# Performance work log

Hardware: AMD Instinct MI355X
Metric: run time of the kernel (lower is better)

## Reference

```python
import jax, jax.numpy as jnp
import numpy as np

B = 16384
N_NARR = 128
N_SUB = 1024
K = N_SUB // N_NARR  # narrative i -> subnarratives [i*K, (i+1)*K)
GAMMA = 2.0
NW, SW, HW = 1.0, 1.0, 0.5  # narrative/subnarrative/hierarchy weights


def setup_inputs() -> dict:
    key = jax.random.key(0)
    k1, k2, k3, k4 = jax.random.split(key, 4)
    return {
        "narrative_logits": jax.random.normal(k1, (B, N_NARR), jnp.float32),
        "subnarrative_logits": jax.random.normal(k2, (B, N_SUB), jnp.float32),
        "narrative_labels": jax.random.randint(k3, (B, N_NARR), 0, 2, jnp.int32),
        "subnarrative_labels": jax.random.randint(k4, (B, N_SUB), 0, 2, jnp.int32),
    }


def _weighted_bce(logits, labels, pos_weight):
    # BCEWithLogits with pos_weight: pw*y*softplus(-x) + (1-y)*softplus(x)
    return pos_weight * labels * jax.nn.softplus(-logits) + (1.0 - labels) * jax.nn.softplus(logits)


def reference(narrative_logits, subnarrative_logits, narrative_labels, subnarrative_labels):
    nl = narrative_labels.astype(jnp.float32)
    sl = subnarrative_labels.astype(jnp.float32)
    b = narrative_logits.shape[0]

    # class-balanced pos_weights, clamped to [1, 50]
    npw = jnp.clip((1.0 - nl).sum(0) / (nl.sum(0) + 1e-6), 1.0, 50.0)
    spw = jnp.clip((1.0 - sl).sum(0) / (sl.sum(0) + 1e-6), 1.0, 50.0)

    narrative_loss = _weighted_bce(narrative_logits, nl, npw).mean()

    # ragged subnarrative loss, vectorized: groups of K subnarrs per narrative.
    # per-(sample, positive-narrative) mean BCE over the group, averaged over
    # the number of valid (sample, narrative) pairs -- same math as the loop.
    sub_bce = _weighted_bce(subnarrative_logits, sl, spw).reshape(b, N_NARR, K)
    per_group = sub_bce.mean(-1)              # [B, N_NARR]
    pos = nl                                   # positive-narrative mask [B, N_NARR]
    valid_count = pos.sum()
    subnarrative_loss = jnp.where(
        valid_count > 0, (per_group * pos).sum() / jnp.maximum(valid_count, 1.0), 0.0)

    # hierarchy consistency: relu(max subnarr prob - narr prob) over positives
    nprob = jax.nn.sigmoid(narrative_logits)
    sprob = jax.nn.sigmoid(subnarrative_logits)
    grp_max = sprob.reshape(b, N_NARR, K).max(-1)  # [B, N_NARR]
    hierarchy_loss = (jax.nn.relu(grp_max - nprob) * pos).sum() / b

    # focal terms (mean over all elements)
    nf = ((1.0 - nprob) ** GAMMA * nl * jax.nn.log_sigmoid(narrative_logits)).mean()
    sf = ((1.0 - sprob) ** GAMMA * sl * jax.nn.log_sigmoid(subnarrative_logits)).mean()

    total = (NW * (narrative_loss - 0.1 * nf)
             + SW * (subnarrative_loss - 0.1 * sf)
             + HW * hierarchy_loss)
    return total
```

## Files before the change

### kernel.cpp

```cpp
#include <hip/hip_runtime.h>


#define BDIM 256
#define NROWS 16384
#define NNARR 128
#define NSUB 1024

#define WS_AN    0
#define WS_CN    128
#define WS_NSUM  256
#define WS_AS    384
#define WS_CS    1408
#define WS_SSUM  2432
#define WS_FN    3456
#define WS_FS    3457
#define WS_HIER  3458
#define WS_FLOATS 3459
#define CSTRIDE  3472

#define NCHUNK 32

__device__ __forceinline__ void bce_pieces(float x, float& sp_p, float& sp_m, float& sig) {
    float a = fabsf(x);
    float e = __expf(-a);
    float l = __logf(1.0f + e);
    sp_p = fmaxf(x, 0.0f) + l;
    sp_m = sp_p - x;
    float inv = __builtin_amdgcn_rcpf(1.0f + e);
    sig = (x >= 0.0f) ? inv : e * inv;
}

template<int RPB>
__global__ __launch_bounds__(BDIM, 6) void ncl_main(
    const float* __restrict__ nlog, const float* __restrict__ slog,
    const int*   __restrict__ nlab, const int*   __restrict__ slab,
    float* __restrict__ P)
{
    __shared__ float sred[BDIM][13];
    __shared__ float ssc[4][3];

    const int t  = threadIdx.x;
    const int r0 = blockIdx.x * RPB;
    float* const Pb = P + (size_t)blockIdx.x * CSTRIDE;

    float fn = 0.f, fs = 0.f, hier = 0.f;

    {
        float An[4] = {0,0,0,0}, Cn[4] = {0,0,0,0}, ns[4] = {0,0,0,0};
        #pragma unroll
        for (int i = 0; i < RPB / 8; ++i) {
            const int base = r0 * NNARR + 4 * (i * BDIM + t);
            const float4 xs = *(const float4*)(nlog + base);
            const int4   ys = *(const int4*)  (nlab + base);
            const float xv[4] = {xs.x, xs.y, xs.z, xs.w};
            const float yv[4] = {(float)ys.x, (float)ys.y, (float)ys.z, (float)ys.w};
            #pragma unroll
            for (int j = 0; j < 4; ++j) {
                float sp_p, sp_m, sig;
                bce_pieces(xv[j], sp_p, sp_m, sig);
                float y = yv[j];
                An[j] += y * sp_m;
                Cn[j] += (1.0f - y) * sp_p;
                ns[j] += y;
                float om = 1.0f - sig;
                fn += om * om * y * (-sp_m);
            }
        }
        #pragma unroll
        for (int j = 0; j < 4; ++j) {
            sred[t][j] = An[j]; sred[t][4 + j] = Cn[j]; sred[t][8 + j] = ns[j];
        }
    }
    __syncthreads();
    if (t < 32) {
        float a[12];
        #pragma unroll
        for (int j = 0; j < 12; ++j) a[j] = sred[t][j];
        #pragma unroll
        for (int s = 1; s < 8; ++s)
            #pragma unroll
            for (int j = 0; j < 12; ++j) a[j] += sred[t + 32 * s][j];
        *(float4*)(Pb + WS_AN   + 4 * t) = make_float4(a[0], a[1], a[2],  a[3]);
        *(float4*)(Pb + WS_CN   + 4 * t) = make_float4(a[4], a[5], a[6],  a[7]);
        *(float4*)(Pb + WS_NSUM + 4 * t) = make_float4(a[8], a[9], a[10], a[11]);
    }

    const int g = t >> 1;
    float As[4] = {0,0,0,0}, Cs[4] = {0,0,0,0}, ss[4] = {0,0,0,0};
    #pragma unroll 4
    for (int i = 0; i < RPB; ++i) {
        const int r = r0 + i;
        const float  nx   = nlog[r * NNARR + g];
        const float  posv = (float)nlab[r * NNARR + g];
        const float4 xs = *(const float4*)(slog + (size_t)r * NSUB + 4 * t);
        const int4   ys = *(const int4*)  (slab + (size_t)r * NSUB + 4 * t);

        float nsig;
        {
            float a = fabsf(nx);
            float e = __expf(-a);
            float inv = __builtin_amdgcn_rcpf(1.0f + e);
            nsig = (nx >= 0.0f) ? inv : e * inv;
        }

        const float xv[4] = {xs.x, xs.y, xs.z, xs.w};
        const float yv[4] = {(float)ys.x, (float)ys.y, (float)ys.z, (float)ys.w};
        float mymax = 0.0f;
        #pragma unroll
        for (int j = 0; j < 4; ++j) {
            float sp_p, sp_m, sig;
            bce_pieces(xv[j], sp_p, sp_m, sig);
            float y = yv[j];
            As[j] += posv * y * sp_m;
            Cs[j] += posv * (1.0f - y) * sp_p;
            ss[j] += y;
            float om = 1.0f - sig;
            fs += om * om * y * (-sp_m);
            mymax = fmaxf(mymax, sig);
        }
        float gmax = fmaxf(mymax, __shfl_xor(mymax, 1, 64));
        if ((t & 1) == 0)
            hier += fmaxf(gmax - nsig, 0.0f) * posv;
    }

    *(float4*)(Pb + WS_AS   + 4 * t) = make_float4(As[0], As[1], As[2], As[3]);
    *(float4*)(Pb + WS_CS   + 4 * t) = make_float4(Cs[0], Cs[1], Cs[2], Cs[3]);
    *(float4*)(Pb + WS_SSUM + 4 * t) = make_float4(ss[0], ss[1], ss[2], ss[3]);

    #pragma unroll
    for (int off = 32; off; off >>= 1) {
        fn   += __shfl_down(fn,   off, 64);
        fs   += __shfl_down(fs,   off, 64);
        hier += __shfl_down(hier, off, 64);
    }
    if ((t & 63) == 0) {
        int w = t >> 6;
        ssc[w][0] = fn; ssc[w][1] = fs; ssc[w][2] = hier;
    }
    __syncthreads();
    if (t == 0) {
        float a = 0.f, b = 0.f, c = 0.f;
        #pragma unroll
        for (int w = 0; w < 4; ++w) { a += ssc[w][0]; b += ssc[w][1]; c += ssc[w][2]; }
        Pb[WS_FN] = a; Pb[WS_FS] = b; Pb[WS_HIER] = c;
    }
}

__global__ __launch_bounds__(256) void ncl_reduce1(const float* __restrict__ P,
                                                   float* __restrict__ tmp,
                                                   int tpg)
{
    const int e = blockIdx.x * 256 + threadIdx.x;
    if (e >= WS_FLOATS) return;
    const int g = blockIdx.y;
    const float* p = P + (size_t)g * tpg * CSTRIDE + e;
    float s = 0.f;
    #pragma unroll 4
    for (int i = 0; i < tpg; ++i)
        s += p[(size_t)i * CSTRIDE];
    tmp[(size_t)g * CSTRIDE + e] = s;
}

__global__ __launch_bounds__(1024) void ncl_finalize(const float* __restrict__ tmp,
                                                     float* __restrict__ out)
{
    __shared__ float sr[6][16];
    const int t = threadIdx.x;
    const float Bf = (float)NROWS;

    float As = 0.f, Csv = 0.f, ss = 0.f;
    #pragma unroll 4
    for (int gc = 0; gc < NCHUNK; ++gc) {
        const float* p = tmp + (size_t)gc * CSTRIDE;
        As  += p[WS_AS   + t];
        Csv += p[WS_CS   + t];
        ss  += p[WS_SSUM + t];
    }
    float spw = fminf(fmaxf((Bf - ss) / (ss + 1e-6f), 1.0f), 50.0f);
    float sub_part = spw * As + Csv;

    float narr_part = 0.f, valid_part = 0.f;
    if (t < NNARR) {
        float An = 0.f, Cn = 0.f, ns = 0.f;
        #pragma unroll 4
        for (int gc = 0; gc < NCHUNK; ++gc) {
            const float* p = tmp + (size_t)gc * CSTRIDE;
            An += p[WS_AN + t]; Cn += p[WS_CN + t]; ns += p[WS_NSUM + t];
        }
        float npw = fminf(fmaxf((Bf - ns) / (ns + 1e-6f), 1.0f), 50.0f);
        narr_part  = npw * An + Cn;
        valid_part = ns;
    }

    float fn_p = 0.f, fs_p = 0.f, hier_p = 0.f;
    if (t < NCHUNK) {
        const float* p = tmp + (size_t)t * CSTRIDE;
        fn_p = p[WS_FN]; fs_p = p[WS_FS]; hier_p = p[WS_HIER];
    }

    #pragma unroll
    for (int off = 32; off; off >>= 1) {
        sub_part   += __shfl_down(sub_part,   off, 64);
        narr_part  += __shfl_down(narr_part,  off, 64);
        valid_part += __shfl_down(valid_part, off, 64);
        fn_p       += __shfl_down(fn_p,       off, 64);
        fs_p       += __shfl_down(fs_p,       off, 64);
        hier_p     += __shfl_down(hier_p,     off, 64);
    }
    if ((t & 63) == 0) {
        int w = t >> 6;
        sr[0][w] = sub_part; sr[1][w] = narr_part; sr[2][w] = valid_part;
        sr[3][w] = fn_p;     sr[4][w] = fs_p;      sr[5][w] = hier_p;
    }
    __syncthreads();
    if (t == 0) {
        float sub_tot = 0.f, narr_tot = 0.f, valid = 0.f;
        float fn = 0.f, fs = 0.f, hier = 0.f;
        #pragma unroll
        for (int i = 0; i < 16; ++i) {
            sub_tot += sr[0][i]; narr_tot += sr[1][i]; valid += sr[2][i];
            fn += sr[3][i]; fs += sr[4][i]; hier += sr[5][i];
        }

        float narrative_loss = narr_tot / (Bf * (float)NNARR);
        float sub_loss = (valid > 0.0f) ? (sub_tot * (1.0f / 8.0f)) / fmaxf(valid, 1.0f) : 0.0f;
        float nf = fn / (Bf * (float)NNARR);
        float sf = fs / (Bf * (float)NSUB);
        float hier_loss = hier / Bf;

        out[0] = (narrative_loss - 0.1f * nf)
               + (sub_loss       - 0.1f * sf)
               + 0.5f * hier_loss;
    }
}

extern "C" void kernel_launch(void* const* d_in, const int* in_sizes, int n_in,
                              void* d_out, int out_size, void* d_ws, size_t ws_size,
                              hipStream_t stream) {
    const float* nlog = (const float*)d_in[0];
    const float* slog = (const float*)d_in[1];
    const int*   nlab = (const int*)d_in[2];
    const int*   slab = (const int*)d_in[3];
    float* P   = (float*)d_ws;
    float* out = (float*)d_out;

    const size_t availf = ws_size / 4;
    const bool big = availf >= (size_t)(2048 + NCHUNK) * CSTRIDE;
    const int nblocks = big ? 2048 : 1024;
    float* tmp = P + (size_t)nblocks * CSTRIDE;
    const int tpg = nblocks / NCHUNK;

    if (big)
        ncl_main<8><<<2048, BDIM, 0, stream>>>(nlog, slog, nlab, slab, P);
    else
        ncl_main<16><<<1024, BDIM, 0, stream>>>(nlog, slog, nlab, slab, P);

    dim3 gr((WS_FLOATS + 255) / 256, NCHUNK);
    ncl_reduce1<<<gr, 256, 0, stream>>>(P, tmp, tpg);
    ncl_finalize<<<1, 1024, 0, stream>>>(tmp, out);
}
```

Measured before the change: 186.3 us.

## Fuse narrative loss into per-row loop and batch four-row loads per iteration

The separate narrative-loss pass, along with its shared-memory reduction and barrier, is folded into the subnarrative row loop. Each even thread now computes the narrative BCE and focal terms for its group from the narrative logit it already loads. Each iteration issues loads for four rows up front to keep more memory requests in flight, and the grid is fixed at 1024 blocks of 16 rows with occupancy hint 4. This drops the redundant narrative transcendental work and the LDS reduction, at the cost of higher register pressure and less parallelism than the 2048-block path.

```diff
diff --git a/kernel.cpp b/kernel.cpp
--- a/kernel.cpp
+++ b/kernel.cpp
@@ -5,6 +5,8 @@
 #define NROWS 16384
 #define NNARR 128
 #define NSUB 1024
+#define RPB 16
+#define NBLOCKS (NROWS / RPB)
 
 #define WS_AN    0
 #define WS_CN    128
@@ -18,7 +20,8 @@
 #define WS_FLOATS 3459
 #define CSTRIDE  3472
 
-#define NCHUNK 32
+#define NCHUNK 16
+#define TPG (NBLOCKS / NCHUNK)
 
 __device__ __forceinline__ void bce_pieces(float x, float& sp_p, float& sp_m, float& sig) {
     float a = fabsf(x);
@@ -30,102 +33,92 @@
     sig = (x >= 0.0f) ? inv : e * inv;
 }
 
-template<int RPB>
-__global__ __launch_bounds__(BDIM, 6) void ncl_main(
+__device__ __forceinline__ void row_accum(
+    const float4 xs, const int4 ys, float nx, float posv, int t,
+    float As[4], float Cs[4], float ss[4],
+    float& An, float& Cn, float& ns, float& fn, float& fs, float& hier)
+{
+    float nsp_p, nsp_m, nsig;
+    bce_pieces(nx, nsp_p, nsp_m, nsig);
+
+    const float xv[4] = {xs.x, xs.y, xs.z, xs.w};
+    const float yv[4] = {(float)ys.x, (float)ys.y, (float)ys.z, (float)ys.w};
+    float mymax = 0.0f;
+    #pragma unroll
+    for (int k = 0; k < 4; ++k) {
+        float sp_p, sp_m, sig;
+        bce_pieces(xv[k], sp_p, sp_m, sig);
+        float y = yv[k];
+        As[k] += posv * y * sp_m;
+        Cs[k] += posv * (1.0f - y) * sp_p;
+        ss[k] += y;
+        float om = 1.0f - sig;
+        fs += om * om * y * (-sp_m);
+        mymax = fmaxf(mymax, sig);
+    }
+    float gmax = fmaxf(mymax, __shfl_xor(mymax, 1, 64));
+    if ((t & 1) == 0) {
+        hier += fmaxf(gmax - nsig, 0.0f) * posv;
+        An += posv * nsp_m;
+        Cn += (1.0f - posv) * nsp_p;
+        ns += posv;
+        float om = 1.0f - nsig;
+        fn += om * om * posv * (-nsp_m);
+    }
+}
+
+__global__ __launch_bounds__(BDIM, 4) void ncl_main(
     const float* __restrict__ nlog, const float* __restrict__ slog,
     const int*   __restrict__ nlab, const int*   __restrict__ slab,
     float* __restrict__ P)
 {
-    __shared__ float sred[BDIM][13];
     __shared__ float ssc[4][3];
 
     const int t  = threadIdx.x;
+    const int g  = t >> 1;
     const int r0 = blockIdx.x * RPB;
     float* const Pb = P + (size_t)blockIdx.x * CSTRIDE;
 
-    float fn = 0.f, fs = 0.f, hier = 0.f;
-
-    {
-        float An[4] = {0,0,0,0}, Cn[4] = {0,0,0,0}, ns[4] = {0,0,0,0};
-        #pragma unroll
-        for (int i = 0; i < RPB / 8; ++i) {
-            const int base = r0 * NNARR + 4 * (i * BDIM + t);
-            const float4 xs = *(const float4*)(nlog + base);
-            const int4   ys = *(const int4*)  (nlab + base);
-            const float xv[4] = {xs.x, xs.y, xs.z, xs.w};
-            const float yv[4] = {(float)ys.x, (float)ys.y, (float)ys.z, (float)ys.w};
-            #pragma unroll
-            for (int j = 0; j < 4; ++j) {
-                float sp_p, sp_m, sig;
-                bce_pieces(xv[j], sp_p, sp_m, sig);
-                float y = yv[j];
-                An[j] += y * sp_m;
-                Cn[j] += (1.0f - y) * sp_p;
-                ns[j] += y;
-                float om = 1.0f - sig;
-                fn += om * om * y * (-sp_m);
-            }
+    float As[4] = {0,0,0,0}, Cs[4] = {0,0,0,0}, ss[4] = {0,0,0,0};
+    float An = 0.f, Cn = 0.f, ns = 0.f, fn = 0.f, fs = 0.f, hier = 0.f;
+
+    #pragma unroll
+    for (int ii = 0; ii < RPB / 4; ++ii) {
+        float4 xs0, xs1, xs2, xs3;
+        int4   ys0, ys1, ys2, ys3;
+        float  nx0, nx1, nx2, nx3, pv0, pv1, pv2, pv3;
+        {
+            const int r = r0 + 4 * ii;
+            const float* s0 = slog + (size_t)r * NSUB + 4 * t;
+            const int*   l0 = slab + (size_t)r * NSUB + 4 * t;
+            const float* n0 = nlog + (size_t)r * NNARR + g;
+            const int*   m0 = nlab + (size_t)r * NNARR + g;
+            xs0 = *(const float4*)(s0);
+            xs1 = *(const float4*)(s0 + NSUB);
+            xs2 = *(const float4*)(s0 + 2 * NSUB);
+            xs3 = *(const float4*)(s0 + 3 * NSUB);
+            ys0 = *(const int4*)(l0);
+            ys1 = *(const int4*)(l0 + NSUB);
+            ys2 = *(const int4*)(l0 + 2 * NSUB);
+            ys3 = *(const int4*)(l0 + 3 * NSUB);
+            nx0 = n0[0]; nx1 = n0[NNARR]; nx2 = n0[2 * NNARR]; nx3 = n0[3 * NNARR];
+            pv0 = (float)m0[0];         pv1 = (float)m0[NNARR];
+            pv2 = (float)m0[2 * NNARR]; pv3 = (float)m0[3 * NNARR];
         }
-        #pragma unroll
-        for (int j = 0; j < 4; ++j) {
-            sred[t][j] = An[j]; sred[t][4 + j] = Cn[j]; sred[t][8 + j] = ns[j];
-        }
-    }
-    __syncthreads();
-    if (t < 32) {
-        float a[12];
-        #pragma unroll
-        for (int j = 0; j < 12; ++j) a[j] = sred[t][j];
-        #pragma unroll
-        for (int s = 1; s < 8; ++s)
-            #pragma unroll
-            for (int j = 0; j < 12; ++j) a[j] += sred[t + 32 * s][j];
-        *(float4*)(Pb + WS_AN   + 4 * t) = make_float4(a[0], a[1], a[2],  a[3]);
-        *(float4*)(Pb + WS_CN   + 4 * t) = make_float4(a[4], a[5], a[6],  a[7]);
-        *(float4*)(Pb + WS_NSUM + 4 * t) = make_float4(a[8], a[9], a[10], a[11]);
-    }
-
-    const int g = t >> 1;
-    float As[4] = {0,0,0,0}, Cs[4] = {0,0,0,0}, ss[4] = {0,0,0,0};
-    #pragma unroll 4
-    for (int i = 0; i < RPB; ++i) {
-        const int r = r0 + i;
-        const float  nx   = nlog[r * NNARR + g];
-        const float  posv = (float)nlab[r * NNARR + g];
-        const float4 xs = *(const float4*)(slog + (size_t)r * NSUB + 4 * t);
-        const int4   ys = *(const int4*)  (slab + (size_t)r * NSUB + 4 * t);
-
-        float nsig;
-        {
-            float a = fabsf(nx);
-            float e = __expf(-a);
-            float inv = __builtin_amdgcn_rcpf(1.0f + e);
-            nsig = (nx >= 0.0f) ? inv : e * inv;
-        }
-
-        const float xv[4] = {xs.x, xs.y, xs.z, xs.w};
-        const float yv[4] = {(float)ys.x, (float)ys.y, (float)ys.z, (float)ys.w};
-        float mymax = 0.0f;
-        #pragma unroll
-        for (int j = 0; j < 4; ++j) {
-            float sp_p, sp_m, sig;
-            bce_pieces(xv[j], sp_p, sp_m, sig);
-            float y = yv[j];
-            As[j] += posv * y * sp_m;
-            Cs[j] += posv * (1.0f - y) * sp_p;
-            ss[j] += y;
-            float om = 1.0f - sig;
-            fs += om * om * y * (-sp_m);
-            mymax = fmaxf(mymax, sig);
-        }
-        float gmax = fmaxf(mymax, __shfl_xor(mymax, 1, 64));
-        if ((t & 1) == 0)
-            hier += fmaxf(gmax - nsig, 0.0f) * posv;
+        row_accum(xs0, ys0, nx0, pv0, t, As, Cs, ss, An, Cn, ns, fn, fs, hier);
+        row_accum(xs1, ys1, nx1, pv1, t, As, Cs, ss, An, Cn, ns, fn, fs, hier);
+        row_accum(xs2, ys2, nx2, pv2, t, As, Cs, ss, An, Cn, ns, fn, fs, hier);
+        row_accum(xs3, ys3, nx3, pv3, t, As, Cs, ss, An, Cn, ns, fn, fs, hier);
     }
 
     *(float4*)(Pb + WS_AS   + 4 * t) = make_float4(As[0], As[1], As[2], As[3]);
     *(float4*)(Pb + WS_CS   + 4 * t) = make_float4(Cs[0], Cs[1], Cs[2], Cs[3]);
     *(float4*)(Pb + WS_SSUM + 4 * t) = make_float4(ss[0], ss[1], ss[2], ss[3]);
+    if ((t & 1) == 0) {
+        Pb[WS_AN   + g] = An;
+        Pb[WS_CN   + g] = Cn;
+        Pb[WS_NSUM + g] = ns;
+    }
 
     #pragma unroll
     for (int off = 32; off; off >>= 1) {
@@ -147,18 +140,17 @@
 }
 
 __global__ __launch_bounds__(256) void ncl_reduce1(const float* __restrict__ P,
-                                                   float* __restrict__ tmp,
-                                                   int tpg)
+                                                   float* __restrict__ tmp)
 {
     const int e = blockIdx.x * 256 + threadIdx.x;
     if (e >= WS_FLOATS) return;
-    const int g = blockIdx.y;
-    const float* p = P + (size_t)g * tpg * CSTRIDE + e;
+    const int gg = blockIdx.y;
+    const float* p = P + (size_t)gg * TPG * CSTRIDE + e;
     float s = 0.f;
     #pragma unroll 4
-    for (int i = 0; i < tpg; ++i)
+    for (int i = 0; i < TPG; ++i)
         s += p[(size_t)i * CSTRIDE];
-    tmp[(size_t)g * CSTRIDE + e] = s;
+    tmp[(size_t)gg * CSTRIDE + e] = s;
 }
 
 __global__ __launch_bounds__(1024) void ncl_finalize(const float* __restrict__ tmp,
@@ -242,20 +234,11 @@
     const int*   nlab = (const int*)d_in[2];
     const int*   slab = (const int*)d_in[3];
     float* P   = (float*)d_ws;
+    float* tmp = P + (size_t)NBLOCKS * CSTRIDE;
     float* out = (float*)d_out;
 
-    const size_t availf = ws_size / 4;
-    const bool big = availf >= (size_t)(2048 + NCHUNK) * CSTRIDE;
-    const int nblocks = big ? 2048 : 1024;
-    float* tmp = P + (size_t)nblocks * CSTRIDE;
-    const int tpg = nblocks / NCHUNK;
-
-    if (big)
-        ncl_main<8><<<2048, BDIM, 0, stream>>>(nlog, slog, nlab, slab, P);
-    else
-        ncl_main<16><<<1024, BDIM, 0, stream>>>(nlog, slog, nlab, slab, P);
-
+    ncl_main<<<NBLOCKS, BDIM, 0, stream>>>(nlog, slog, nlab, slab, P);
     dim3 gr((WS_FLOATS + 255) / 256, NCHUNK);
-    ncl_reduce1<<<gr, 256, 0, stream>>>(P, tmp, tpg);
+    ncl_reduce1<<<gr, 256, 0, stream>>>(P, tmp);
     ncl_finalize<<<1, 1024, 0, stream>>>(tmp, out);
 }
```

New measurement: 322.2 us. 1.73x slower.
